# Optimization experiments

Hardware: AMD Instinct MI355X
Metric: run time of the kernel (lower is better)

The kernel has to match this reference:

```python
import jax, jax.numpy as jnp
import numpy as np

D_MODEL = 768
NUM_HEADS = 12
D_HEAD = D_MODEL // NUM_HEADS
LN_EPS = 1e-5


def layer_norm(x, w, b):
    m = jnp.mean(x, axis=-1, keepdims=True)
    v = jnp.mean(jnp.square(x - m), axis=-1, keepdims=True)
    return (x - m) * jax.lax.rsqrt(v + LN_EPS) * w + b


def setup_inputs() -> dict:
    key = jax.random.key(0)
    ks = jax.random.split(key, 10)
    B, P, NQ, D = 16, 197, 8, D_MODEL
    s = 1.0 / np.sqrt(D)
    return {
        "q_x": jax.random.normal(ks[0], (1, NQ, D), jnp.float32),
        "kv_x": jax.random.normal(ks[1], (B, P, D), jnp.float32),
        "pair_pos_embedding": jax.random.normal(ks[2], (2 * P, D), jnp.float32) * 0.02,
        "q_w": jax.random.normal(ks[3], (D, D), jnp.float32) * s,
        "q_b": jnp.zeros((D,), jnp.float32),
        "kv_w": jax.random.normal(ks[4], (D, D), jnp.float32) * s,
        "kv_b": jnp.zeros((D,), jnp.float32),
        "out_w": jax.random.normal(ks[5], (D, D), jnp.float32) * s,
        "out_b": jnp.zeros((D,), jnp.float32),
        "lnq_w": jnp.ones((D,), jnp.float32),
        "lnq_b": jnp.zeros((D,), jnp.float32),
        "lnkv_w": jnp.ones((D,), jnp.float32),
        "lnkv_b": jnp.zeros((D,), jnp.float32),
    }


def reference(q_x, kv_x, pair_pos_embedding, q_w, q_b, kv_w, kv_b,
              out_w, out_b, lnq_w, lnq_b, lnkv_w, lnkv_b):
    H, dh = NUM_HEADS, D_HEAD
    scale = dh ** -0.5
    _, NQ, D = q_x.shape
    B, P, _ = kv_x.shape

    # q path: Linear -> LN -> split heads -> [1, H, NQ, dh]
    q = layer_norm(q_x @ q_w.T + q_b, lnq_w, lnq_b)
    q = q.reshape(1, NQ, H, dh).transpose(0, 2, 1, 3)  # [1,H,NQ,dh]

    # kv path: Linear -> LN -> split heads -> [B, H, P, dh]
    kv = layer_norm(kv_x @ kv_w.T + kv_b, lnkv_w, lnkv_b)
    kv = kv.reshape(B, P, H, dh).transpose(0, 2, 1, 3)  # [B,H,P,dh]

    # pairwise expansion: kv_concat[i*B+j] = cat(kv[i], kv[j]) along token dim
    kv_rep = jnp.repeat(kv, B, axis=0)          # [B^2,H,P,dh] (repeat_interleave)
    kv_til = jnp.tile(kv, (B, 1, 1, 1))         # [B^2,H,P,dh]
    kv_cat = jnp.concatenate([kv_rep, kv_til], axis=2)  # [B^2,H,2P,dh]

    # positional bias: [2P, D] -> [1, H, 2P, dh]
    pos = pair_pos_embedding.reshape(1, 2 * P, H, dh).transpose(0, 2, 1, 3)
    kv_cat = kv_cat + pos

    scores = jnp.einsum('bhqd,bhpd->bhqp', jnp.broadcast_to(q, (B * B, H, NQ, dh)), kv_cat) * scale
    attn = jax.nn.softmax(scores, axis=-1)      # [B^2,H,NQ,2P]

    v1 = jnp.einsum('bhqp,bhpd->bhqd', attn[..., :P], kv_cat[:, :, :P, :])
    v2 = jnp.einsum('bhqp,bhpd->bhqd', attn[..., P:], kv_cat[:, :, P:, :])
    values = (v1 - v2).transpose(0, 2, 1, 3).reshape(B * B, NQ, D)
    return values @ out_w.T + out_b
```

## Files before the change

kernel.cpp:

```cpp
#include <hip/hip_runtime.h>
#include <hip/hip_bf16.h>
#include <math.h>

#define D_MODEL 768
#define NHEADS  12
#define DHEAD   64
#define NQR     8
#define BB      16
#define PP      197
#define NPAIR   256
#define MKV     (BB*PP)
#define LN_EPSF 1e-5f
#define SCALEF  0.125f

#define KTOT  2304
#define KSPLIT 3
#define KPER  (KTOT/KSPLIT)
#define MPAD  3200
#define BM 128
#define BN 128
#define BK 64

typedef __attribute__((ext_vector_type(8))) short short8v;
typedef __attribute__((ext_vector_type(4))) float float4v;

__device__ __forceinline__ void gload16(const void* g, void* l){
  __builtin_amdgcn_global_load_lds(
      (const __attribute__((address_space(1))) unsigned int*)g,
      (__attribute__((address_space(3))) unsigned int*)l, 16, 0, 0);
}

__global__ __launch_bounds__(256) void qgemm_kernel(
    const float* __restrict__ qx, const float* __restrict__ qw,
    float* __restrict__ qy)
{
  __shared__ float xs[NQR*D_MODEL];
  int tid = threadIdx.x;
  for (int e = tid*4; e < NQR*D_MODEL; e += 1024)
    *(float4*)&xs[e] = *(const float4*)&qx[e];
  __syncthreads();
  int col = tid >> 5, lane = tid & 31;
  int c = blockIdx.x*8 + col;
  const float* wr = qw + (size_t)c*D_MODEL;
  float acc[NQR] = {};
  for (int k = lane*4; k < D_MODEL; k += 128){
    float4 w4 = *(const float4*)&wr[k];
    #pragma unroll
    for (int q = 0; q < NQR; q++){
      float4 x4 = *(const float4*)&xs[q*D_MODEL + k];
      acc[q] += x4.x*w4.x + x4.y*w4.y + x4.z*w4.z + x4.w*w4.w;
    }
  }
  #pragma unroll
  for (int q = 0; q < NQR; q++){
    float a = acc[q];
    for (int off = 16; off >= 1; off >>= 1) a += __shfl_xor(a, off, 32);
    if (lane == 0) qy[q*D_MODEL + c] = a;
  }
}

__global__ __launch_bounds__(256) void ln_rows_kernel(
    const float* __restrict__ Y, const float* __restrict__ bias,
    const float* __restrict__ lnw, const float* __restrict__ lnb,
    float* __restrict__ out)
{
  __shared__ float red[256], red2[256];
  int r = blockIdx.x, tid = threadIdx.x;
  const float* yr = Y + (size_t)r*D_MODEL;
  float x0 = yr[tid      ] + bias[tid      ];
  float x1 = yr[tid + 256] + bias[tid + 256];
  float x2 = yr[tid + 512] + bias[tid + 512];
  red[tid] = x0 + x1 + x2; red2[tid] = x0*x0 + x1*x1 + x2*x2;
  __syncthreads();
  for (int st = 128; st > 0; st >>= 1){
    if (tid < st){ red[tid] += red[tid+st]; red2[tid] += red2[tid+st]; }
    __syncthreads();
  }
  float mean = red[0]*(1.f/768.f);
  float var  = red2[0]*(1.f/768.f) - mean*mean;
  float inv  = rsqrtf(var + LN_EPSF);
  float* orow = out + (size_t)r*D_MODEL;
  orow[tid      ] = (x0-mean)*inv*lnw[tid      ] + lnb[tid      ];
  orow[tid + 256] = (x1-mean)*inv*lnw[tid + 256] + lnb[tid + 256];
  orow[tid + 512] = (x2-mean)*inv*lnw[tid + 512] + lnb[tid + 512];
}

__global__ __launch_bounds__(192) void pack_both_kernel(
    const float* __restrict__ kvx, const float* __restrict__ kvw,
    __hip_bfloat16* __restrict__ Ab, __hip_bfloat16* __restrict__ Wb)
{
  int b = blockIdx.x, t = threadIdx.x;
  const float* X; __hip_bfloat16* Y; int valid, mode, m;
  if (b < MPAD){ X = kvx; Y = Ab; valid = MKV;     mode = 0; m = b; }
  else         { X = kvw; Y = Wb; valid = D_MODEL; mode = 1; m = b - MPAD; }
  int k = t*4;
  float4 v = (m < valid) ? *(const float4*)&X[(size_t)m*D_MODEL + k]
                         : make_float4(0.f,0.f,0.f,0.f);
  float xsv[4] = {v.x, v.y, v.z, v.w};
  unsigned short hu[4], lu[4];
  #pragma unroll
  for (int i = 0; i < 4; i++){
    __hip_bfloat16 h = __float2bfloat16(xsv[i]);
    float hf = __bfloat162float(h);
    __hip_bfloat16 l = __float2bfloat16(xsv[i] - hf);
    hu[i] = *(unsigned short*)&h;
    lu[i] = *(unsigned short*)&l;
  }
  ushort4 hv = {hu[0], hu[1], hu[2], hu[3]};
  ushort4 lv = {lu[0], lu[1], lu[2], lu[3]};
  ushort4* row = (ushort4*)(Y + (size_t)m*KTOT);
  int s = k >> 2;
  if (mode == 0){ row[s] = hv; row[s+192] = hv; row[s+384] = lv; }
  else          { row[s] = hv; row[s+192] = lv; row[s+384] = hv; }
}

__global__ __launch_bounds__(256) void gemm_mfma_kernel(
    const __hip_bfloat16* __restrict__ Ab, const __hip_bfloat16* __restrict__ Wb,
    float* __restrict__ Cp)
{
  __shared__ __hip_bfloat16 As[BM*BK];
  __shared__ __hip_bfloat16 Bs[BN*BK];
  int tid = threadIdx.x;
  int wave = tid >> 6, lane = tid & 63;
  int m0 = blockIdx.x*BM, n0 = blockIdx.y*BN, kt = blockIdx.z;
  int wr = wave >> 1, wc = wave & 1;

  float4v acc[4][4];
  #pragma unroll
  for (int i = 0; i < 4; i++)
    #pragma unroll
    for (int j = 0; j < 4; j++)
      acc[i][j] = (float4v){0.f, 0.f, 0.f, 0.f};

  int sbase = wave*256;
  for (int st = 0; st < KPER/BK; ++st){
    int k0 = kt*KPER + st*BK;
    __syncthreads();
    #pragma unroll
    for (int i = 0; i < 4; i++){
      int s  = sbase + i*64 + lane;
      int r  = s >> 3, kg = s & 7;
      int kgg = kg ^ (r & 7);
      gload16(Ab + (size_t)(m0 + r)*KTOT + k0 + kgg*8, (char*)As + (size_t)s*16);
      gload16(Wb + (size_t)(n0 + r)*KTOT + k0 + kgg*8, (char*)Bs + (size_t)s*16);
    }
    __syncthreads();
    #pragma unroll
    for (int ks = 0; ks < 2; ks++){
      int kq = ks*4 + (lane >> 4);
      short8v af[4], bf[4];
      #pragma unroll
      for (int t = 0; t < 4; t++){
        int ar = wr*64 + t*16 + (lane & 15);
        int as_ = ar*8 + (kq ^ (ar & 7));
        af[t] = *(const short8v*)((const char*)As + (size_t)as_*16);
        int br = wc*64 + t*16 + (lane & 15);
        int bs_ = br*8 + (kq ^ (br & 7));
        bf[t] = *(const short8v*)((const char*)Bs + (size_t)bs_*16);
      }
      #pragma unroll
      for (int i = 0; i < 4; i++)
        #pragma unroll
        for (int j = 0; j < 4; j++)
          acc[i][j] = __builtin_amdgcn_mfma_f32_16x16x32_bf16(af[i], bf[j], acc[i][j], 0, 0, 0);
    }
  }

  float* C = Cp + (size_t)kt*MKV*D_MODEL;
  #pragma unroll
  for (int i = 0; i < 4; i++){
    int mb = m0 + wr*64 + i*16 + ((lane >> 4) << 2);
    #pragma unroll
    for (int j = 0; j < 4; j++){
      int n = n0 + wc*64 + j*16 + (lane & 15);
      #pragma unroll
      for (int r = 0; r < 4; r++){
        int m = mb + r;
        if (m < MKV) C[(size_t)m*D_MODEL + n] = acc[i][j][r];
      }
    }
  }
}

__global__ __launch_bounds__(256) void ln_rows3_kernel(
    const float* __restrict__ Y0, const float* __restrict__ Y1,
    const float* __restrict__ Y2, const float* __restrict__ bias,
    const float* __restrict__ lnw, const float* __restrict__ lnb,
    float* __restrict__ out)
{
  __shared__ float red[256], red2[256];
  int r = blockIdx.x, tid = threadIdx.x;
  const float* y0 = Y0 + (size_t)r*D_MODEL;
  const float* y1 = Y1 + (size_t)r*D_MODEL;
  const float* y2 = Y2 + (size_t)r*D_MODEL;
  float x0 = y0[tid      ] + y1[tid      ] + y2[tid      ] + bias[tid      ];
  float x1 = y0[tid + 256] + y1[tid + 256] + y2[tid + 256] + bias[tid + 256];
  float x2 = y0[tid + 512] + y1[tid + 512] + y2[tid + 512] + bias[tid + 512];
  red[tid] = x0 + x1 + x2; red2[tid] = x0*x0 + x1*x1 + x2*x2;
  __syncthreads();
  for (int st = 128; st > 0; st >>= 1){
    if (tid < st){ red[tid] += red[tid+st]; red2[tid] += red2[tid+st]; }
    __syncthreads();
  }
  float mean = red[0]*(1.f/768.f);
  float var  = red2[0]*(1.f/768.f) - mean*mean;
  float inv  = rsqrtf(var + LN_EPSF);
  float* orow = out + (size_t)r*D_MODEL;
  orow[tid      ] = (x0-mean)*inv*lnw[tid      ] + lnb[tid      ];
  orow[tid + 256] = (x1-mean)*inv*lnw[tid + 256] + lnb[tid + 256];
  orow[tid + 512] = (x2-mean)*inv*lnw[tid + 512] + lnb[tid + 512];
}

__global__ __launch_bounds__(256) void rank_proj_kernel(
    const float* __restrict__ kv_ln, const float* __restrict__ q_ln,
    const float* __restrict__ ppe, const float* __restrict__ ow,
    float* __restrict__ m1O, float* __restrict__ z1O,
    float* __restrict__ m2O, float* __restrict__ z2O,
    float* __restrict__ p1, float* __restrict__ p2)
{
  __shared__ float A[PP*65];
  __shared__ float qs[NQR*64];
  __shared__ float E[NQR*PP];
  __shared__ float Us[16*64];
  int r = blockIdx.x, h = blockIdx.y;
  int tid = threadIdx.x;

  for (int e = tid; e < NQR*64; e += 256){
    int q = e >> 6, d = e & 63;
    qs[e] = q_ln[q*D_MODEL + h*64 + d];
  }

  for (int half = 0; half < 2; half++){
    __syncthreads();
    for (int e = tid; e < PP*64; e += 256){
      int p = e >> 6, d = e & 63;
      A[p*65 + d] = kv_ln[((size_t)(r*PP + p))*D_MODEL + h*64 + d]
                  + ppe[((size_t)(half*PP + p))*D_MODEL + h*64 + d];
    }
    __syncthreads();

    int q = tid >> 5, sub = tid & 31;
    float s[7];
    #pragma unroll
    for (int i = 0; i < 7; i++) s[i] = 0.f;
    for (int d = 0; d < 64; d++){
      float qv = qs[q*64 + d];
      #pragma unroll
      for (int i = 0; i < 7; i++){
        int p = sub + 32*i;
        int pc = p < PP ? p : PP-1;
        s[i] += qv * A[pc*65 + d];
      }
    }
    float mloc = -1e30f;
    #pragma unroll
    for (int i = 0; i < 7; i++){
      int p = sub + 32*i;
      s[i] = (p < PP) ? s[i]*SCALEF : -1e30f;
      mloc = fmaxf(mloc, s[i]);
    }
    for (int off = 16; off >= 1; off >>= 1)
      mloc = fmaxf(mloc, __shfl_xor(mloc, off, 32));
    float zloc = 0.f;
    #pragma unroll
    for (int i = 0; i < 7; i++){
      int p = sub + 32*i;
      float e = __expf(s[i] - mloc);
      if (p < PP){ E[q*PP + p] = e; zloc += e; }
    }
    for (int off = 16; off >= 1; off >>= 1)
      zloc += __shfl_xor(zloc, off, 32);

    int idx = (r*NHEADS + h)*NQR + q;
    if (sub == 0){
      if (half){ m2O[idx] = mloc; z2O[idx] = zloc; }
      else     { m1O[idx] = mloc; z1O[idx] = zloc; }
    }
    __syncthreads();

    float u0 = 0.f, u1 = 0.f;
    for (int p = 0; p < PP; p++){
      float e = E[q*PP + p];
      u0 += e * A[p*65 + sub];
      u1 += e * A[p*65 + sub + 32];
    }
    Us[(half*NQR + q)*64 + sub]      = u0;
    Us[(half*NQR + q)*64 + sub + 32] = u1;
  }
  __syncthreads();

  float acc[16][3];
  #pragma unroll
  for (int m = 0; m < 16; m++){ acc[m][0]=0.f; acc[m][1]=0.f; acc[m][2]=0.f; }
  const float* owh = ow + h*64;
  for (int d4 = 0; d4 < 64; d4 += 4){
    float4 w0 = *(const float4*)&owh[(size_t)(tid      )*D_MODEL + d4];
    float4 w1 = *(const float4*)&owh[(size_t)(tid + 256)*D_MODEL + d4];
    float4 w2 = *(const float4*)&owh[(size_t)(tid + 512)*D_MODEL + d4];
    #pragma unroll
    for (int m = 0; m < 16; m++){
      float4 u = *(const float4*)&Us[m*64 + d4];
      acc[m][0] += u.x*w0.x + u.y*w0.y + u.z*w0.z + u.w*w0.w;
      acc[m][1] += u.x*w1.x + u.y*w1.y + u.z*w1.z + u.w*w1.w;
      acc[m][2] += u.x*w2.x + u.y*w2.y + u.z*w2.z + u.w*w2.w;
    }
  }
  #pragma unroll
  for (int q = 0; q < NQR; q++){
    size_t base = (((size_t)r*NHEADS + h)*NQR + q)*D_MODEL;
    #pragma unroll
    for (int j = 0; j < 3; j++){
      p1[base + tid + 256*j] = acc[q][j];
      p2[base + tid + 256*j] = acc[8 + q][j];
    }
  }
}

__global__ __launch_bounds__(256) void combine_out_kernel(
    const float* __restrict__ m1, const float* __restrict__ z1,
    const float* __restrict__ m2, const float* __restrict__ z2,
    const float* __restrict__ p1, const float* __restrict__ p2,
    const float* __restrict__ out_b, float* __restrict__ out)
{
  __shared__ float c1s[NHEADS], c2s[NHEADS];
  int pair = blockIdx.x, q = blockIdx.y, tid = threadIdx.x;
  int i = pair >> 4, j = pair & 15;
  if (tid < NHEADS){
    int h = tid;
    int ii = (i*NHEADS + h)*NQR + q;
    int jj = (j*NHEADS + h)*NQR + q;
    float mi = m1[ii], mj = m2[jj];
    float mm = fmaxf(mi, mj);
    float a1 = __expf(mi - mm), a2 = __expf(mj - mm);
    float rden = 1.f / (a1*z1[ii] + a2*z2[jj]);
    c1s[h] = a1*rden; c2s[h] = a2*rden;
  }
  __syncthreads();
  float* orow = out + ((size_t)(pair*NQR + q))*D_MODEL;
  for (int nn = tid; nn < D_MODEL; nn += 256){
    float acc = out_b[nn];
    #pragma unroll
    for (int h = 0; h < NHEADS; h++){
      acc += c1s[h]*p1[(((size_t)i*NHEADS + h)*NQR + q)*D_MODEL + nn]
           - c2s[h]*p2[(((size_t)j*NHEADS + h)*NQR + q)*D_MODEL + nn];
    }
    orow[nn] = acc;
  }
}

extern "C" void kernel_launch(void* const* d_in, const int* in_sizes, int n_in,
                              void* d_out, int out_size, void* d_ws, size_t ws_size,
                              hipStream_t stream)
{
  const float* q_x    = (const float*)d_in[0];
  const float* kv_x   = (const float*)d_in[1];
  const float* ppe    = (const float*)d_in[2];
  const float* q_w    = (const float*)d_in[3];
  const float* q_b    = (const float*)d_in[4];
  const float* kv_w   = (const float*)d_in[5];
  const float* kv_b   = (const float*)d_in[6];
  const float* out_w  = (const float*)d_in[7];
  const float* out_b  = (const float*)d_in[8];
  const float* lnq_w  = (const float*)d_in[9];
  const float* lnq_b  = (const float*)d_in[10];
  const float* lnkv_w = (const float*)d_in[11];
  const float* lnkv_b = (const float*)d_in[12];
  float* out = (float*)d_out;

  float* ws    = (float*)d_ws;
  float* q_y   = ws;
  float* q_ln  = q_y  + NQR*D_MODEL;
  float* Abuf_f = q_ln + NQR*D_MODEL;
  float* Wbuf_f = Abuf_f + (size_t)MPAD*KTOT/2;
  float* C0    = Wbuf_f + (size_t)D_MODEL*KTOT/2;
  float* C1    = C0 + (size_t)MKV*D_MODEL;
  float* C2    = C1 + (size_t)MKV*D_MODEL;

  __hip_bfloat16* Abuf = (__hip_bfloat16*)Abuf_f;
  __hip_bfloat16* Wbuf = (__hip_bfloat16*)Wbuf_f;

  float* kv_ln = Abuf_f;
  float* m1    = Wbuf_f;
  float* z1    = m1 + BB*NHEADS*NQR;
  float* m2    = z1 + BB*NHEADS*NQR;
  float* z2    = m2 + BB*NHEADS*NQR;
  float* p1    = C0;
  float* p2    = p1 + (size_t)BB*NHEADS*NQR*D_MODEL;

  qgemm_kernel<<<96, 256, 0, stream>>>(q_x, q_w, q_y);
  ln_rows_kernel<<<NQR, 256, 0, stream>>>(q_y, q_b, lnq_w, lnq_b, q_ln);

  pack_both_kernel<<<MPAD + D_MODEL, 192, 0, stream>>>(kv_x, kv_w, Abuf, Wbuf);

  gemm_mfma_kernel<<<dim3(MPAD/BM, D_MODEL/BN, KSPLIT), 256, 0, stream>>>(
      Abuf, Wbuf, C0);

  ln_rows3_kernel<<<MKV, 256, 0, stream>>>(C0, C1, C2, kv_b, lnkv_w, lnkv_b, kv_ln);

  rank_proj_kernel<<<dim3(BB, NHEADS), 256, 0, stream>>>(
      kv_ln, q_ln, ppe, out_w, m1, z1, m2, z2, p1, p2);

  combine_out_kernel<<<dim3(NPAIR, NQR), 256, 0, stream>>>(
      m1, z1, m2, z2, p1, p2, out_b, out);
}
```

Measured before the change: 180.9 us.

## Split rank_proj halves across grid and transpose K tile with swizzled LDS

The rank_proj kernel now launches a third grid dimension for the two token halves instead of looping over them in one block, doubling block count from 192 to 384. Each block handles one half, so it needs only half the Us buffer and half the output-projection accumulators. It also stores the K tile transposed with an XOR swizzle, so the weighted-sum loop can read float4 vectors of E and K without bank conflicts. The cost is that each block reloads the query and reads the out_w slice again, and the smem tile grows to 64x256 floats.

```diff
diff --git a/kernel.cpp b/kernel.cpp
--- a/kernel.cpp
+++ b/kernel.cpp
@@ -211,6 +211,12 @@
   orow[tid + 512] = (x2-mean)*inv*lnw[tid + 512] + lnb[tid + 512];
 }
 
+#define ATS 256
+#define EPS_ 208
+__device__ __forceinline__ int at_idx(int d, int p){
+  return d*ATS + ((((p >> 2) ^ (d & 7)) << 2) | (p & 3));
+}
+
 __global__ __launch_bounds__(256) void rank_proj_kernel(
     const float* __restrict__ kv_ln, const float* __restrict__ q_ln,
     const float* __restrict__ ppe, const float* __restrict__ ow,
@@ -218,101 +224,103 @@
     float* __restrict__ m2O, float* __restrict__ z2O,
     float* __restrict__ p1, float* __restrict__ p2)
 {
-  __shared__ float A[PP*65];
+  __shared__ float AT[64*ATS];
   __shared__ float qs[NQR*64];
-  __shared__ float E[NQR*PP];
-  __shared__ float Us[16*64];
-  int r = blockIdx.x, h = blockIdx.y;
+  __shared__ float E[NQR*EPS_];
+  __shared__ float Us[NQR*64];
+  int r = blockIdx.x, h = blockIdx.y, half = blockIdx.z;
   int tid = threadIdx.x;
 
   for (int e = tid; e < NQR*64; e += 256){
     int q = e >> 6, d = e & 63;
     qs[e] = q_ln[q*D_MODEL + h*64 + d];
   }
-
-  for (int half = 0; half < 2; half++){
-    __syncthreads();
-    for (int e = tid; e < PP*64; e += 256){
-      int p = e >> 6, d = e & 63;
-      A[p*65 + d] = kv_ln[((size_t)(r*PP + p))*D_MODEL + h*64 + d]
-                  + ppe[((size_t)(half*PP + p))*D_MODEL + h*64 + d];
-    }
-    __syncthreads();
-
-    int q = tid >> 5, sub = tid & 31;
-    float s[7];
-    #pragma unroll
-    for (int i = 0; i < 7; i++) s[i] = 0.f;
-    for (int d = 0; d < 64; d++){
-      float qv = qs[q*64 + d];
-      #pragma unroll
-      for (int i = 0; i < 7; i++){
-        int p = sub + 32*i;
-        int pc = p < PP ? p : PP-1;
-        s[i] += qv * A[pc*65 + d];
-      }
-    }
-    float mloc = -1e30f;
+  for (int e = tid; e < 200*64; e += 256){
+    int p = e >> 6, d = e & 63;
+    float v = 0.f;
+    if (p < PP)
+      v = kv_ln[((size_t)(r*PP + p))*D_MODEL + h*64 + d]
+        + ppe[((size_t)(half*PP + p))*D_MODEL + h*64 + d];
+    AT[at_idx(d, p)] = v;
+  }
+  __syncthreads();
+
+  int q = tid >> 5, sub = tid & 31;
+  float s[7];
+  #pragma unroll
+  for (int i = 0; i < 7; i++) s[i] = 0.f;
+  for (int d = 0; d < 64; d++){
+    float qv = qs[q*64 + d];
     #pragma unroll
     for (int i = 0; i < 7; i++){
       int p = sub + 32*i;
-      s[i] = (p < PP) ? s[i]*SCALEF : -1e30f;
-      mloc = fmaxf(mloc, s[i]);
-    }
-    for (int off = 16; off >= 1; off >>= 1)
-      mloc = fmaxf(mloc, __shfl_xor(mloc, off, 32));
-    float zloc = 0.f;
-    #pragma unroll
-    for (int i = 0; i < 7; i++){
-      int p = sub + 32*i;
-      float e = __expf(s[i] - mloc);
-      if (p < PP){ E[q*PP + p] = e; zloc += e; }
-    }
-    for (int off = 16; off >= 1; off >>= 1)
-      zloc += __shfl_xor(zloc, off, 32);
-
-    int idx = (r*NHEADS + h)*NQR + q;
-    if (sub == 0){
-      if (half){ m2O[idx] = mloc; z2O[idx] = zloc; }
-      else     { m1O[idx] = mloc; z1O[idx] = zloc; }
-    }
-    __syncthreads();
-
-    float u0 = 0.f, u1 = 0.f;
-    for (int p = 0; p < PP; p++){
-      float e = E[q*PP + p];
-      u0 += e * A[p*65 + sub];
-      u1 += e * A[p*65 + sub + 32];
-    }
-    Us[(half*NQR + q)*64 + sub]      = u0;
-    Us[(half*NQR + q)*64 + sub + 32] = u1;
-  }
-  __syncthreads();
-
-  float acc[16][3];
-  #pragma unroll
-  for (int m = 0; m < 16; m++){ acc[m][0]=0.f; acc[m][1]=0.f; acc[m][2]=0.f; }
+      int pc = p < PP ? p : PP-1;
+      s[i] += qv * AT[at_idx(d, pc)];
+    }
+  }
+  float mloc = -1e30f;
+  #pragma unroll
+  for (int i = 0; i < 7; i++){
+    int p = sub + 32*i;
+    s[i] = (p < PP) ? s[i]*SCALEF : -1e30f;
+    mloc = fmaxf(mloc, s[i]);
+  }
+  for (int off = 16; off >= 1; off >>= 1)
+    mloc = fmaxf(mloc, __shfl_xor(mloc, off, 32));
+  float zloc = 0.f;
+  #pragma unroll
+  for (int i = 0; i < 7; i++){
+    int p = sub + 32*i;
+    float e = __expf(s[i] - mloc);
+    if (p < PP){ E[q*EPS_ + p] = e; zloc += e; }
+    else if (p < 200){ E[q*EPS_ + p] = 0.f; }
+  }
+  for (int off = 16; off >= 1; off >>= 1)
+    zloc += __shfl_xor(zloc, off, 32);
+
+  int idx = (r*NHEADS + h)*NQR + q;
+  if (sub == 0){
+    if (half){ m2O[idx] = mloc; z2O[idx] = zloc; }
+    else     { m1O[idx] = mloc; z1O[idx] = zloc; }
+  }
+
+  float u0 = 0.f, u1 = 0.f;
+  int sw = (sub & 7);
+  for (int p4 = 0; p4 < 200; p4 += 4){
+    float4 e4 = *(const float4*)&E[q*EPS_ + p4];
+    int cb = (((p4 >> 2) ^ sw) << 2);
+    float4 a0 = *(const float4*)&AT[sub*ATS + cb];
+    float4 a1 = *(const float4*)&AT[(sub+32)*ATS + cb];
+    u0 += e4.x*a0.x + e4.y*a0.y + e4.z*a0.z + e4.w*a0.w;
+    u1 += e4.x*a1.x + e4.y*a1.y + e4.z*a1.z + e4.w*a1.w;
+  }
+  Us[q*64 + sub]      = u0;
+  Us[q*64 + sub + 32] = u1;
+  __syncthreads();
+
+  float acc[NQR][3];
+  #pragma unroll
+  for (int m = 0; m < NQR; m++){ acc[m][0]=0.f; acc[m][1]=0.f; acc[m][2]=0.f; }
   const float* owh = ow + h*64;
   for (int d4 = 0; d4 < 64; d4 += 4){
     float4 w0 = *(const float4*)&owh[(size_t)(tid      )*D_MODEL + d4];
     float4 w1 = *(const float4*)&owh[(size_t)(tid + 256)*D_MODEL + d4];
     float4 w2 = *(const float4*)&owh[(size_t)(tid + 512)*D_MODEL + d4];
     #pragma unroll
-    for (int m = 0; m < 16; m++){
+    for (int m = 0; m < NQR; m++){
       float4 u = *(const float4*)&Us[m*64 + d4];
       acc[m][0] += u.x*w0.x + u.y*w0.y + u.z*w0.z + u.w*w0.w;
       acc[m][1] += u.x*w1.x + u.y*w1.y + u.z*w1.z + u.w*w1.w;
       acc[m][2] += u.x*w2.x + u.y*w2.y + u.z*w2.z + u.w*w2.w;
     }
   }
-  #pragma unroll
-  for (int q = 0; q < NQR; q++){
-    size_t base = (((size_t)r*NHEADS + h)*NQR + q)*D_MODEL;
-    #pragma unroll
-    for (int j = 0; j < 3; j++){
-      p1[base + tid + 256*j] = acc[q][j];
-      p2[base + tid + 256*j] = acc[8 + q][j];
-    }
+  float* P = half ? p2 : p1;
+  #pragma unroll
+  for (int m = 0; m < NQR; m++){
+    size_t base = (((size_t)r*NHEADS + h)*NQR + m)*D_MODEL;
+    #pragma unroll
+    for (int j = 0; j < 3; j++)
+      P[base + tid + 256*j] = acc[m][j];
   }
 }
 
@@ -397,7 +405,7 @@
 
   ln_rows3_kernel<<<MKV, 256, 0, stream>>>(C0, C1, C2, kv_b, lnkv_w, lnkv_b, kv_ln);
 
-  rank_proj_kernel<<<dim3(BB, NHEADS), 256, 0, stream>>>(
+  rank_proj_kernel<<<dim3(BB, NHEADS, 2), 256, 0, stream>>>(
       kv_ln, q_ln, ppe, out_w, m1, z1, m2, z2, p1, p2);
 
   combine_out_kernel<<<dim3(NPAIR, NQR), 256, 0, stream>>>(
```

New measurement: 189.2 us. +4.6%, slower.

## Split rank attention into token-chunked blocks with flash-style merge before projection

Applied to the files above, without the earlier changes.

The single per-(batch,head) kernel that looped over both halves of 197 tokens is replaced by one kernel that handles each half and each of two token chunks in separate blocks, writing partial max, sum and weighted values. A second kernel merges the chunk partials with online-softmax rescaling and runs the output projection per half. This raises the block count from 192 to 768 for the attention part and shrinks shared memory per block to fill more CUs. In exchange it adds a kernel launch and a global round-trip for the partial results, and each merge block re-reads the out_w slice.

```diff
diff --git a/kernel.cpp b/kernel.cpp
--- a/kernel.cpp
+++ b/kernel.cpp
@@ -20,6 +20,13 @@
 #define BM 128
 #define BN 128
 #define BK 64
+
+#define NCHUNK 2
+#define CH0    100
+#define CH1    97
+#define CHMAX  100
+#define EROW   104
+#define NIDX   (BB*NHEADS*2*NQR)
 
 typedef __attribute__((ext_vector_type(8))) short short8v;
 typedef __attribute__((ext_vector_type(4))) float float4v;
@@ -211,108 +218,138 @@
   orow[tid + 512] = (x2-mean)*inv*lnw[tid + 512] + lnb[tid + 512];
 }
 
-__global__ __launch_bounds__(256) void rank_proj_kernel(
+__global__ __launch_bounds__(256) void rank_chunk_kernel(
     const float* __restrict__ kv_ln, const float* __restrict__ q_ln,
-    const float* __restrict__ ppe, const float* __restrict__ ow,
+    const float* __restrict__ ppe,
+    float* __restrict__ mC, float* __restrict__ zC, float* __restrict__ UC)
+{
+  __shared__ float A[CHMAX*65];
+  __shared__ float qs[NQR*64];
+  __shared__ float E[NQR*EROW];
+  int r = blockIdx.x, h = blockIdx.y;
+  int half = blockIdx.z >> 1, c = blockIdx.z & 1;
+  int p0 = c ? CH0 : 0;
+  int np = c ? CH1 : CH0;
+  int tid = threadIdx.x;
+
+  for (int e = tid; e < NQR*64; e += 256){
+    int q = e >> 6, d = e & 63;
+    qs[e] = q_ln[q*D_MODEL + h*64 + d];
+  }
+  for (int e = tid; e < np*16; e += 256){
+    int p = e >> 4, dq = (e & 15) << 2;
+    float4 a = *(const float4*)&kv_ln[((size_t)(r*PP + p0 + p))*D_MODEL + h*64 + dq];
+    float4 b = *(const float4*)&ppe[((size_t)(half*PP + p0 + p))*D_MODEL + h*64 + dq];
+    float* row = &A[p*65 + dq];
+    row[0] = a.x + b.x; row[1] = a.y + b.y;
+    row[2] = a.z + b.z; row[3] = a.w + b.w;
+  }
+  __syncthreads();
+
+  int q = tid >> 5, sub = tid & 31;
+  float s[4];
+  #pragma unroll
+  for (int i = 0; i < 4; i++) s[i] = 0.f;
+  for (int d = 0; d < 64; d++){
+    float qv = qs[q*64 + d];
+    #pragma unroll
+    for (int i = 0; i < 4; i++){
+      int p = sub + 32*i;
+      int pc = p < np ? p : np-1;
+      s[i] += qv * A[pc*65 + d];
+    }
+  }
+  float mloc = -1e30f;
+  #pragma unroll
+  for (int i = 0; i < 4; i++){
+    int p = sub + 32*i;
+    s[i] = (p < np) ? s[i]*SCALEF : -1e30f;
+    mloc = fmaxf(mloc, s[i]);
+  }
+  for (int off = 16; off >= 1; off >>= 1)
+    mloc = fmaxf(mloc, __shfl_xor(mloc, off, 32));
+  float zloc = 0.f;
+  #pragma unroll
+  for (int i = 0; i < 4; i++){
+    int p = sub + 32*i;
+    float e = __expf(s[i] - mloc);
+    if (p < np){ E[q*EROW + p] = e; zloc += e; }
+  }
+  for (int off = 16; off >= 1; off >>= 1)
+    zloc += __shfl_xor(zloc, off, 32);
+
+  int idx = (((r*NHEADS + h)*2 + half)*NQR + q);
+  if (sub == 0){
+    mC[c*NIDX + idx] = mloc;
+    zC[c*NIDX + idx] = zloc;
+  }
+
+  float u0 = 0.f, u1 = 0.f;
+  for (int p = 0; p < np; p++){
+    float e = E[q*EROW + p];
+    u0 += e * A[p*65 + sub];
+    u1 += e * A[p*65 + sub + 32];
+  }
+  float* urow = UC + ((size_t)(c*NIDX + idx))*64;
+  urow[sub]      = u0;
+  urow[sub + 32] = u1;
+}
+
+__global__ __launch_bounds__(256) void merge_proj_kernel(
+    const float* __restrict__ mC, const float* __restrict__ zC,
+    const float* __restrict__ UC, const float* __restrict__ ow,
     float* __restrict__ m1O, float* __restrict__ z1O,
     float* __restrict__ m2O, float* __restrict__ z2O,
     float* __restrict__ p1, float* __restrict__ p2)
 {
-  __shared__ float A[PP*65];
-  __shared__ float qs[NQR*64];
-  __shared__ float E[NQR*PP];
-  __shared__ float Us[16*64];
-  int r = blockIdx.x, h = blockIdx.y;
+  __shared__ float Us[NQR*64];
+  __shared__ float a0s[NQR], a1s[NQR];
+  int r = blockIdx.x, h = blockIdx.y, half = blockIdx.z;
   int tid = threadIdx.x;
-
+  int base = (((r*NHEADS + h)*2 + half)*NQR);
+
+  if (tid < NQR){
+    int q = tid;
+    float m0 = mC[base + q],        m1v = mC[NIDX + base + q];
+    float z0 = zC[base + q],        z1v = zC[NIDX + base + q];
+    float mm = fmaxf(m0, m1v);
+    float a0 = __expf(m0 - mm), a1 = __expf(m1v - mm);
+    a0s[q] = a0; a1s[q] = a1;
+    int oidx = (r*NHEADS + h)*NQR + q;
+    if (half){ m2O[oidx] = mm; z2O[oidx] = a0*z0 + a1*z1v; }
+    else     { m1O[oidx] = mm; z1O[oidx] = a0*z0 + a1*z1v; }
+  }
+  __syncthreads();
   for (int e = tid; e < NQR*64; e += 256){
-    int q = e >> 6, d = e & 63;
-    qs[e] = q_ln[q*D_MODEL + h*64 + d];
-  }
-
-  for (int half = 0; half < 2; half++){
-    __syncthreads();
-    for (int e = tid; e < PP*64; e += 256){
-      int p = e >> 6, d = e & 63;
-      A[p*65 + d] = kv_ln[((size_t)(r*PP + p))*D_MODEL + h*64 + d]
-                  + ppe[((size_t)(half*PP + p))*D_MODEL + h*64 + d];
-    }
-    __syncthreads();
-
-    int q = tid >> 5, sub = tid & 31;
-    float s[7];
-    #pragma unroll
-    for (int i = 0; i < 7; i++) s[i] = 0.f;
-    for (int d = 0; d < 64; d++){
-      float qv = qs[q*64 + d];
-      #pragma unroll
-      for (int i = 0; i < 7; i++){
-        int p = sub + 32*i;
-        int pc = p < PP ? p : PP-1;
-        s[i] += qv * A[pc*65 + d];
-      }
-    }
-    float mloc = -1e30f;
-    #pragma unroll
-    for (int i = 0; i < 7; i++){
-      int p = sub + 32*i;
-      s[i] = (p < PP) ? s[i]*SCALEF : -1e30f;
-      mloc = fmaxf(mloc, s[i]);
-    }
-    for (int off = 16; off >= 1; off >>= 1)
-      mloc = fmaxf(mloc, __shfl_xor(mloc, off, 32));
-    float zloc = 0.f;
-    #pragma unroll
-    for (int i = 0; i < 7; i++){
-      int p = sub + 32*i;
-      float e = __expf(s[i] - mloc);
-      if (p < PP){ E[q*PP + p] = e; zloc += e; }
-    }
-    for (int off = 16; off >= 1; off >>= 1)
-      zloc += __shfl_xor(zloc, off, 32);
-
-    int idx = (r*NHEADS + h)*NQR + q;
-    if (sub == 0){
-      if (half){ m2O[idx] = mloc; z2O[idx] = zloc; }
-      else     { m1O[idx] = mloc; z1O[idx] = zloc; }
-    }
-    __syncthreads();
-
-    float u0 = 0.f, u1 = 0.f;
-    for (int p = 0; p < PP; p++){
-      float e = E[q*PP + p];
-      u0 += e * A[p*65 + sub];
-      u1 += e * A[p*65 + sub + 32];
-    }
-    Us[(half*NQR + q)*64 + sub]      = u0;
-    Us[(half*NQR + q)*64 + sub + 32] = u1;
-  }
-  __syncthreads();
-
-  float acc[16][3];
-  #pragma unroll
-  for (int m = 0; m < 16; m++){ acc[m][0]=0.f; acc[m][1]=0.f; acc[m][2]=0.f; }
+    int q = e >> 6;
+    Us[e] = a0s[q]*UC[((size_t)(base))*64 + e]
+          + a1s[q]*UC[((size_t)(NIDX + base))*64 + e];
+  }
+  __syncthreads();
+
+  float acc[NQR][3];
+  #pragma unroll
+  for (int m = 0; m < NQR; m++){ acc[m][0]=0.f; acc[m][1]=0.f; acc[m][2]=0.f; }
   const float* owh = ow + h*64;
   for (int d4 = 0; d4 < 64; d4 += 4){
     float4 w0 = *(const float4*)&owh[(size_t)(tid      )*D_MODEL + d4];
     float4 w1 = *(const float4*)&owh[(size_t)(tid + 256)*D_MODEL + d4];
     float4 w2 = *(const float4*)&owh[(size_t)(tid + 512)*D_MODEL + d4];
     #pragma unroll
-    for (int m = 0; m < 16; m++){
+    for (int m = 0; m < NQR; m++){
       float4 u = *(const float4*)&Us[m*64 + d4];
       acc[m][0] += u.x*w0.x + u.y*w0.y + u.z*w0.z + u.w*w0.w;
       acc[m][1] += u.x*w1.x + u.y*w1.y + u.z*w1.z + u.w*w1.w;
       acc[m][2] += u.x*w2.x + u.y*w2.y + u.z*w2.z + u.w*w2.w;
     }
   }
-  #pragma unroll
-  for (int q = 0; q < NQR; q++){
-    size_t base = (((size_t)r*NHEADS + h)*NQR + q)*D_MODEL;
-    #pragma unroll
-    for (int j = 0; j < 3; j++){
-      p1[base + tid + 256*j] = acc[q][j];
-      p2[base + tid + 256*j] = acc[8 + q][j];
-    }
+  float* P = half ? p2 : p1;
+  #pragma unroll
+  for (int m = 0; m < NQR; m++){
+    size_t obase = (((size_t)r*NHEADS + h)*NQR + m)*D_MODEL;
+    #pragma unroll
+    for (int j = 0; j < 3; j++)
+      P[obase + tid + 256*j] = acc[m][j];
   }
 }
 
@@ -380,7 +417,10 @@
   __hip_bfloat16* Wbuf = (__hip_bfloat16*)Wbuf_f;
 
   float* kv_ln = Abuf_f;
-  float* m1    = Wbuf_f;
+  float* mC    = Wbuf_f;
+  float* zC    = mC + NCHUNK*NIDX;
+  float* UC    = zC + NCHUNK*NIDX;
+  float* m1    = UC + (size_t)NCHUNK*NIDX*64;
   float* z1    = m1 + BB*NHEADS*NQR;
   float* m2    = z1 + BB*NHEADS*NQR;
   float* z2    = m2 + BB*NHEADS*NQR;
@@ -397,8 +437,11 @@
 
   ln_rows3_kernel<<<MKV, 256, 0, stream>>>(C0, C1, C2, kv_b, lnkv_w, lnkv_b, kv_ln);
 
-  rank_proj_kernel<<<dim3(BB, NHEADS), 256, 0, stream>>>(
-      kv_ln, q_ln, ppe, out_w, m1, z1, m2, z2, p1, p2);
+  rank_chunk_kernel<<<dim3(BB, NHEADS, 4), 256, 0, stream>>>(
+      kv_ln, q_ln, ppe, mC, zC, UC);
+
+  merge_proj_kernel<<<dim3(BB, NHEADS, 2), 256, 0, stream>>>(
+      mC, zC, UC, out_w, m1, z1, m2, z2, p1, p2);
 
   combine_out_kernel<<<dim3(NPAIR, NQR), 256, 0, stream>>>(
       m1, z1, m2, z2, p1, p2, out_b, out);
```

Result: no change. 178.5 us (-1.3%).
